# Performance work log

Measured on AMD Instinct MI355X. Metric: run time of the kernel, lower is better.

## Reference

```python
import jax, jax.numpy as jnp
import numpy as np

NUM_CAPS = 32
OUT_DIM = 8   # capsule vector length in channel terms; note the view() below mixes spatial dims
H_OUT = 6
W_OUT = 6


def setup_inputs() -> dict:
    key = jax.random.key(0)
    k1, k2, k3 = jax.random.split(key, 3)
    X = jax.random.normal(k1, (512, 256, 20, 20), dtype=jnp.float32)
    # 32 Conv2d(256->8, k=9) stacked capsule-major into one grouped-output conv
    W = jax.random.normal(k2, (256, 256, 9, 9), dtype=jnp.float32) * 0.02
    b = jax.random.normal(k3, (256,), dtype=jnp.float32) * 0.02
    return {"X": X, "W": W, "b": b}


def squash(u):
    # u: [B, 1152, 8]; squash along last dim (matches torch code exactly)
    ns = jnp.sum(u * u, axis=-1, keepdims=True)
    return ns / (1.0 + ns) * (u / (0.001 + jnp.sqrt(ns)))


def reference(X, W, b):
    # One conv replaces the 32 separate Conv2d modules; output channels are
    # ordered [cap0_ch0..cap0_ch7, cap1_ch0..], identical to torch.stack(dim=1)
    # followed by contiguous view.
    y = jax.lax.conv_general_dilated(
        X, W, window_strides=(2, 2), padding='VALID',
        dimension_numbers=('NCHW', 'OIHW', 'NCHW'))  # [B, 256, 6, 6]
    y = y + b[None, :, None, None]
    B = X.shape[0]
    # torch: stack -> [B,32,8,6,6] -> view(B, 32*36, -1) is a raw contiguous
    # reshape; [B,256,6,6] has the same memory layout, so reshape directly.
    u = y.reshape(B, NUM_CAPS * H_OUT * W_OUT, OUT_DIM)  # [B, 1152, 8]
    return squash(u)
```

## Files before the change

### kernel.cpp

```cpp
#include <hip/hip_runtime.h>
#include <hip/hip_bf16.h>
#include <stdint.h>

typedef __attribute__((ext_vector_type(8))) short bf16x8;
typedef __attribute__((ext_vector_type(4))) float f32x4;

__device__ __forceinline__ unsigned short f2bf(float f) {
  union { float f; unsigned int u; } v; v.f = f;
  unsigned int u = v.u;
  u += 0x7fffu + ((u >> 16) & 1u);
  return (unsigned short)(u >> 16);
}

__global__ __launch_bounds__(256) void xform_x(const float* __restrict__ X,
                                               unsigned short* __restrict__ Xt) {
  const int b = blockIdx.x;
  const int t = threadIdx.x;
  const float* src = X + ((size_t)b * 256 + t) * 400;
  unsigned short* dst = Xt + (size_t)b * 400 * 256 + t;
  for (int hw = 0; hw < 400; hw += 4) {
    float4 v = *(const float4*)(src + hw);
    dst[(size_t)(hw + 0) * 256] = f2bf(v.x);
    dst[(size_t)(hw + 1) * 256] = f2bf(v.y);
    dst[(size_t)(hw + 2) * 256] = f2bf(v.z);
    dst[(size_t)(hw + 3) * 256] = f2bf(v.w);
  }
}

__global__ __launch_bounds__(256) void xform_w(const float* __restrict__ W,
                                               unsigned short* __restrict__ Wt) {
  __shared__ unsigned short lds[81 * 128];
  const int co = blockIdx.x;
  const int ct = blockIdx.y;
  const int t = threadIdx.x;
  const float* src = W + ((size_t)co * 256 + (size_t)ct * 128) * 81;
  for (int idx = t; idx < 128 * 81; idx += 256) {
    int ci_l = idx / 81, khw = idx - ci_l * 81;
    lds[khw * 128 + ci_l] = f2bf(src[idx]);
  }
  __syncthreads();
  unsigned short* dst = Wt + (size_t)co * 256 + (size_t)ct * 128;
  for (int idx = t; idx < 81 * 128; idx += 256) {
    int khw = idx >> 7, ci_l = idx & 127;
    dst[(size_t)khw * 65536 + ci_l] = lds[idx];
  }
}

__device__ __forceinline__ void gload16(const unsigned short* g, unsigned short* l) {
  __builtin_amdgcn_global_load_lds(
      (const __attribute__((address_space(1))) unsigned int*)g,
      (__attribute__((address_space(3))) unsigned int*)l, 16, 0, 0);
}

__global__ __launch_bounds__(256, 2) void conv_gemm(
    const unsigned short* __restrict__ Xt,
    const unsigned short* __restrict__ Wt,
    const float* __restrict__ bias,
    float* __restrict__ Y) {
  __shared__ unsigned short sA[128 * 64];
  __shared__ unsigned short sB[64 * 64];
  const int mt = blockIdx.x;
  const int nt = blockIdx.y;
  const int t = threadIdx.x;
  const int c8 = t & 7, rq = t >> 3;
  const int swz = (c8 ^ (rq & 7)) * 8;

  int xb[4];
  #pragma unroll
  for (int r = 0; r < 4; ++r) {
    int m = mt * 128 + r * 32 + rq;
    int b = m / 36, s = m - b * 36;
    int oh = s / 6, ow = s - oh * 6;
    xb[r] = ((b * 20 + 2 * oh) * 20 + 2 * ow) * 256;
  }
  int wb[2];
  #pragma unroll
  for (int r = 0; r < 2; ++r) wb[r] = (nt * 64 + r * 32 + rq) * 256;

  unsigned short* ldsA = sA + t * 8;
  unsigned short* ldsB = sB + t * 8;

  const int lane = t & 63, wv = t >> 6;
  const int wm = (wv >> 1) * 64, wn = (wv & 1) * 32;
  const int l15 = lane & 15, l4 = lane >> 4, l7 = lane & 7;

  const unsigned short* pA[4][2];
  const unsigned short* pB[2][2];
  #pragma unroll
  for (int i = 0; i < 4; ++i)
    #pragma unroll
    for (int kk = 0; kk < 2; ++kk)
      pA[i][kk] = sA + ((wm + i * 16 + l15) * 128 +
                        ((kk * 64 + l4 * 16) ^ (l7 << 4))) / 2;
  #pragma unroll
  for (int j = 0; j < 2; ++j)
    #pragma unroll
    for (int kk = 0; kk < 2; ++kk)
      pB[j][kk] = sB + ((wn + j * 16 + l15) * 128 +
                        ((kk * 64 + l4 * 16) ^ (l7 << 4))) / 2;

  f32x4 acc[4][2];
  #pragma unroll
  for (int i = 0; i < 4; ++i)
    #pragma unroll
    for (int j = 0; j < 2; ++j) acc[i][j] = (f32x4){0.f, 0.f, 0.f, 0.f};

  #pragma unroll 1
  for (int kh = 0; kh < 9; ++kh) {
    #pragma unroll 1
    for (int kw = 0; kw < 9; ++kw) {
      const unsigned short* xsrc = Xt + (kh * 20 + kw) * 256 + swz;
      const unsigned short* wsrc = Wt + (kh * 9 + kw) * 65536 + swz;
      for (int ci0 = 0; ci0 < 256; ci0 += 64) {
        gload16(xsrc + xb[0] + ci0, ldsA + 0 * 2048);
        gload16(xsrc + xb[1] + ci0, ldsA + 1 * 2048);
        gload16(xsrc + xb[2] + ci0, ldsA + 2 * 2048);
        gload16(xsrc + xb[3] + ci0, ldsA + 3 * 2048);
        gload16(wsrc + wb[0] + ci0, ldsB + 0 * 2048);
        gload16(wsrc + wb[1] + ci0, ldsB + 1 * 2048);
        __syncthreads();
        bf16x8 af[4][2], bfr[2][2];
        #pragma unroll
        for (int i = 0; i < 4; ++i)
          #pragma unroll
          for (int kk = 0; kk < 2; ++kk) af[i][kk] = *(const bf16x8*)pA[i][kk];
        #pragma unroll
        for (int j = 0; j < 2; ++j)
          #pragma unroll
          for (int kk = 0; kk < 2; ++kk) bfr[j][kk] = *(const bf16x8*)pB[j][kk];
        #pragma unroll
        for (int i = 0; i < 4; ++i)
          #pragma unroll
          for (int j = 0; j < 2; ++j) {
            acc[i][j] = __builtin_amdgcn_mfma_f32_16x16x32_bf16(
                af[i][0], bfr[j][0], acc[i][j], 0, 0, 0);
            acc[i][j] = __builtin_amdgcn_mfma_f32_16x16x32_bf16(
                af[i][1], bfr[j][1], acc[i][j], 0, 0, 0);
          }
        __syncthreads();
      }
    }
  }

  #pragma unroll
  for (int j = 0; j < 2; ++j) {
    int co = nt * 64 + wn + j * 16 + l15;
    float bb = bias[co];
    #pragma unroll
    for (int i = 0; i < 4; ++i) {
      int m0 = mt * 128 + wm + i * 16 + l4 * 4;
      #pragma unroll
      for (int q = 0; q < 4; ++q) {
        int m = m0 + q;
        int b = m / 36, s = m - b * 36;
        Y[((size_t)b * 256 + co) * 36 + s] = acc[i][j][q] + bb;
      }
    }
  }
}

__global__ __launch_bounds__(256) void squash_k(float* __restrict__ Y) {
  const int g = blockIdx.x * 256 + threadIdx.x;
  float4* p = (float4*)(Y + (size_t)g * 8);
  float4 a = p[0], b = p[1];
  float ns = a.x * a.x + a.y * a.y + a.z * a.z + a.w * a.w +
             b.x * b.x + b.y * b.y + b.z * b.z + b.w * b.w;
  float sc = ns / ((1.0f + ns) * (0.001f + sqrtf(ns)));
  a.x *= sc; a.y *= sc; a.z *= sc; a.w *= sc;
  b.x *= sc; b.y *= sc; b.z *= sc; b.w *= sc;
  p[0] = a; p[1] = b;
}

extern "C" void kernel_launch(void* const* d_in, const int* in_sizes, int n_in,
                              void* d_out, int out_size, void* d_ws, size_t ws_size,
                              hipStream_t stream) {
  const float* X = (const float*)d_in[0];
  const float* W = (const float*)d_in[1];
  const float* bias = (const float*)d_in[2];
  float* Y = (float*)d_out;

  unsigned short* Xt = (unsigned short*)d_ws;
  unsigned short* Wt = Xt + (size_t)512 * 400 * 256;

  xform_x<<<512, 256, 0, stream>>>(X, Xt);
  xform_w<<<dim3(256, 2), 256, 0, stream>>>(W, Wt);
  conv_gemm<<<dim3(144, 4), 256, 0, stream>>>(Xt, Wt, bias, Y);
  squash_k<<<2304, 256, 0, stream>>>(Y);
}
```

Baseline: 385.0 us.

## Load A fragments directly to registers and double-buffer B in LDS

The conv GEMM no longer stages the activation tile in LDS. Each lane reads its A fragments straight from global memory into registers, which cuts LDS traffic and footprint. The weight tile is double-buffered in LDS and A registers are ping-ponged, so the next k-step's loads are issued before the current MFMAs run. The risk is uncoalesced direct global reads for A and higher register pressure under launch_bounds(256,2).

```diff
diff --git a/kernel.cpp b/kernel.cpp
--- a/kernel.cpp
+++ b/kernel.cpp
@@ -57,89 +57,102 @@
     const unsigned short* __restrict__ Wt,
     const float* __restrict__ bias,
     float* __restrict__ Y) {
-  __shared__ unsigned short sA[128 * 64];
-  __shared__ unsigned short sB[64 * 64];
+  __shared__ unsigned short sB[2 * 64 * 64];
   const int mt = blockIdx.x;
   const int nt = blockIdx.y;
   const int t = threadIdx.x;
   const int c8 = t & 7, rq = t >> 3;
   const int swz = (c8 ^ (rq & 7)) * 8;
 
-  int xb[4];
-  #pragma unroll
-  for (int r = 0; r < 4; ++r) {
-    int m = mt * 128 + r * 32 + rq;
-    int b = m / 36, s = m - b * 36;
-    int oh = s / 6, ow = s - oh * 6;
-    xb[r] = ((b * 20 + 2 * oh) * 20 + 2 * ow) * 256;
-  }
-  int wb[2];
-  #pragma unroll
-  for (int r = 0; r < 2; ++r) wb[r] = (nt * 64 + r * 32 + rq) * 256;
-
-  unsigned short* ldsA = sA + t * 8;
+  const int wb0 = (nt * 64 + rq) * 256 + swz;
+  const int wb1 = (nt * 64 + 32 + rq) * 256 + swz;
   unsigned short* ldsB = sB + t * 8;
 
   const int lane = t & 63, wv = t >> 6;
   const int wm = (wv >> 1) * 64, wn = (wv & 1) * 32;
   const int l15 = lane & 15, l4 = lane >> 4, l7 = lane & 7;
 
-  const unsigned short* pA[4][2];
-  const unsigned short* pB[2][2];
+  int arow[4];
+  #pragma unroll
+  for (int i = 0; i < 4; ++i) {
+    int m = mt * 128 + wm + i * 16 + l15;
+    int b = m / 36, s = m - b * 36;
+    int oh = s / 6, ow = s - oh * 6;
+    arow[i] = ((b * 20 + 2 * oh) * 20 + 2 * ow) * 256 + l4 * 8;
+  }
+
+  int pBo[2][2];
+  #pragma unroll
+  for (int j = 0; j < 2; ++j)
+    #pragma unroll
+    for (int kk = 0; kk < 2; ++kk)
+      pBo[j][kk] = ((wn + j * 16 + l15) * 128 +
+                    ((kk * 64 + l4 * 16) ^ (l7 << 4))) / 2;
+
+  f32x4 acc[4][2];
   #pragma unroll
   for (int i = 0; i < 4; ++i)
     #pragma unroll
-    for (int kk = 0; kk < 2; ++kk)
-      pA[i][kk] = sA + ((wm + i * 16 + l15) * 128 +
-                        ((kk * 64 + l4 * 16) ^ (l7 << 4))) / 2;
-  #pragma unroll
-  for (int j = 0; j < 2; ++j)
-    #pragma unroll
-    for (int kk = 0; kk < 2; ++kk)
-      pB[j][kk] = sB + ((wn + j * 16 + l15) * 128 +
-                        ((kk * 64 + l4 * 16) ^ (l7 << 4))) / 2;
-
-  f32x4 acc[4][2];
-  #pragma unroll
-  for (int i = 0; i < 4; ++i)
-    #pragma unroll
     for (int j = 0; j < 2; ++j) acc[i][j] = (f32x4){0.f, 0.f, 0.f, 0.f};
 
+  bf16x8 afA[4][2], afB[4][2];
+
+  int s_ci = 0, s_kw = 0, xo = 0, wo = 0;
+  auto adv = [&]() {
+    if (s_ci < 3) { ++s_ci; xo += 64; wo += 64; }
+    else {
+      s_ci = 0; wo += 65536 - 192;
+      if (s_kw < 8) { ++s_kw; xo += 64; }
+      else          { s_kw = 0; xo += 2880; }
+    }
+  };
+  auto loadA = [&](bf16x8 (&af)[4][2]) {
+    #pragma unroll
+    for (int i = 0; i < 4; ++i)
+      #pragma unroll
+      for (int kk = 0; kk < 2; ++kk)
+        af[i][kk] = *(const bf16x8*)(Xt + arow[i] + xo + kk * 32);
+  };
+  auto stageB = [&](int bufo) {
+    gload16(Wt + wo + wb0, ldsB + bufo);
+    gload16(Wt + wo + wb1, ldsB + bufo + 2048);
+  };
+  auto compute = [&](const unsigned short* base, bf16x8 (&af)[4][2]) {
+    bf16x8 bfr[2][2];
+    #pragma unroll
+    for (int j = 0; j < 2; ++j)
+      #pragma unroll
+      for (int kk = 0; kk < 2; ++kk)
+        bfr[j][kk] = *(const bf16x8*)(base + pBo[j][kk]);
+    #pragma unroll
+    for (int i = 0; i < 4; ++i)
+      #pragma unroll
+      for (int j = 0; j < 2; ++j) {
+        acc[i][j] = __builtin_amdgcn_mfma_f32_16x16x32_bf16(
+            af[i][0], bfr[j][0], acc[i][j], 0, 0, 0);
+        acc[i][j] = __builtin_amdgcn_mfma_f32_16x16x32_bf16(
+            af[i][1], bfr[j][1], acc[i][j], 0, 0, 0);
+      }
+  };
+
+  stageB(0);
+  loadA(afA);
+  adv();
+
   #pragma unroll 1
-  for (int kh = 0; kh < 9; ++kh) {
-    #pragma unroll 1
-    for (int kw = 0; kw < 9; ++kw) {
-      const unsigned short* xsrc = Xt + (kh * 20 + kw) * 256 + swz;
-      const unsigned short* wsrc = Wt + (kh * 9 + kw) * 65536 + swz;
-      for (int ci0 = 0; ci0 < 256; ci0 += 64) {
-        gload16(xsrc + xb[0] + ci0, ldsA + 0 * 2048);
-        gload16(xsrc + xb[1] + ci0, ldsA + 1 * 2048);
-        gload16(xsrc + xb[2] + ci0, ldsA + 2 * 2048);
-        gload16(xsrc + xb[3] + ci0, ldsA + 3 * 2048);
-        gload16(wsrc + wb[0] + ci0, ldsB + 0 * 2048);
-        gload16(wsrc + wb[1] + ci0, ldsB + 1 * 2048);
-        __syncthreads();
-        bf16x8 af[4][2], bfr[2][2];
-        #pragma unroll
-        for (int i = 0; i < 4; ++i)
-          #pragma unroll
-          for (int kk = 0; kk < 2; ++kk) af[i][kk] = *(const bf16x8*)pA[i][kk];
-        #pragma unroll
-        for (int j = 0; j < 2; ++j)
-          #pragma unroll
-          for (int kk = 0; kk < 2; ++kk) bfr[j][kk] = *(const bf16x8*)pB[j][kk];
-        #pragma unroll
-        for (int i = 0; i < 4; ++i)
-          #pragma unroll
-          for (int j = 0; j < 2; ++j) {
-            acc[i][j] = __builtin_amdgcn_mfma_f32_16x16x32_bf16(
-                af[i][0], bfr[j][0], acc[i][j], 0, 0, 0);
-            acc[i][j] = __builtin_amdgcn_mfma_f32_16x16x32_bf16(
-                af[i][1], bfr[j][1], acc[i][j], 0, 0, 0);
-          }
-        __syncthreads();
-      }
+  for (int s = 0; s < 324; s += 2) {
+    __syncthreads();
+    stageB(4096);
+    loadA(afB);
+    adv();
+    compute(sB, afA);
+    __syncthreads();
+    if (s + 2 < 324) {
+      stageB(0);
+      loadA(afA);
+      adv();
     }
+    compute(sB + 4096, afB);
   }
 
   #pragma unroll
```

Result: slower. 1.171 ms (+204.1%).

## Restructure conv GEMM with double-buffered LDS and intra-block split-K reduction

Applied to the files above, without the earlier changes.

Rewrites the conv GEMM main loop. It now uses a 64x128 tile with a K step of 32 and double-buffered LDS, so the global-to-LDS loads for the next step overlap with the MFMAs on the current one and one barrier per step replaces two. The four waves form two split-K halves over the flattened (kh, kw, ci) range. Their partial accumulators are reduced through LDS before bias is added and the result is stored. Launch bounds go to 3 blocks per CU and the grid becomes 288x2. The cost is extra LDS traffic for the reduction and a smaller K chunk per barrier.

```diff
diff --git a/kernel.cpp b/kernel.cpp
--- a/kernel.cpp
+++ b/kernel.cpp
@@ -52,108 +52,115 @@
       (__attribute__((address_space(3))) unsigned int*)l, 16, 0, 0);
 }
 
-__global__ __launch_bounds__(256, 2) void conv_gemm(
+__global__ __launch_bounds__(256, 3) void conv_gemm(
     const unsigned short* __restrict__ Xt,
     const unsigned short* __restrict__ Wt,
     const float* __restrict__ bias,
     float* __restrict__ Y) {
-  __shared__ unsigned short sA[128 * 64];
-  __shared__ unsigned short sB[64 * 64];
+  __shared__ __align__(16) unsigned short lds[2 * 12288];
   const int mt = blockIdx.x;
   const int nt = blockIdx.y;
   const int t = threadIdx.x;
-  const int c8 = t & 7, rq = t >> 3;
-  const int swz = (c8 ^ (rq & 7)) * 8;
+  const int l = t & 63, w = t >> 6;
+  const int wks = w >> 1;
+  const int l15 = l & 15, l4 = l >> 4;
+  const int sw = (l15 >> 1) & 3;
 
-  int xb[4];
+  int xsrcA[2], destA[2];
+  #pragma unroll
+  for (int r = 0; r < 2; ++r) {
+    int row = (w & 1) * 32 + r * 16 + (l >> 2);
+    int c4s = (l & 3) ^ ((row >> 1) & 3);
+    int m = mt * 64 + row;
+    int b = m / 36, sr = m - b * 36;
+    int oh = sr / 6, ow = sr - oh * 6;
+    xsrcA[r] = ((b * 20 + 2 * oh) * 20 + 2 * ow) * 256 + c4s * 8;
+    destA[r] = (w * 128 + r * 64 + l) * 8;
+  }
+  int wsrcB[4], destB[4];
   #pragma unroll
   for (int r = 0; r < 4; ++r) {
-    int m = mt * 128 + r * 32 + rq;
-    int b = m / 36, s = m - b * 36;
-    int oh = s / 6, ow = s - oh * 6;
-    xb[r] = ((b * 20 + 2 * oh) * 20 + 2 * ow) * 256;
+    int co = (w & 1) * 64 + r * 16 + (l >> 2);
+    int c4s = (l & 3) ^ ((co >> 1) & 3);
+    wsrcB[r] = (nt * 128 + co) * 256 + c4s * 8;
+    destB[r] = 4096 + (w * 256 + r * 64 + l) * 8;
   }
-  int wb[2];
-  #pragma unroll
-  for (int r = 0; r < 2; ++r) wb[r] = (nt * 64 + r * 32 + rq) * 256;
 
-  unsigned short* ldsA = sA + t * 8;
-  unsigned short* ldsB = sB + t * 8;
+  const int aoff = wks * 2048 + l15 * 32 + ((l4 ^ sw) * 8);
+  const int boff = 4096 + wks * 4096 + ((w & 1) * 64 + l15) * 32 + ((l4 ^ sw) * 8);
 
-  const int lane = t & 63, wv = t >> 6;
-  const int wm = (wv >> 1) * 64, wn = (wv & 1) * 32;
-  const int l15 = lane & 15, l4 = lane >> 4, l7 = lane & 7;
-
-  const unsigned short* pA[4][2];
-  const unsigned short* pB[2][2];
+  f32x4 acc[4][4];
   #pragma unroll
   for (int i = 0; i < 4; ++i)
     #pragma unroll
-    for (int kk = 0; kk < 2; ++kk)
-      pA[i][kk] = sA + ((wm + i * 16 + l15) * 128 +
-                        ((kk * 64 + l4 * 16) ^ (l7 << 4))) / 2;
-  #pragma unroll
-  for (int j = 0; j < 2; ++j)
+    for (int j = 0; j < 4; ++j) acc[i][j] = (f32x4){0.f, 0.f, 0.f, 0.f};
+
+  int xo, wo, ci, kw;
+  if (wks == 0) { xo = 0;     wo = 0;       ci = 0; kw = 0; }
+  else          { xo = 21632; wo = 2621568; ci = 4; kw = 4; }
+
+  auto adv = [&]() {
+    if (ci < 7) { ++ci; xo += 32; wo += 32; }
+    else { ci = 0; wo += 65312;
+           if (kw < 8) { ++kw; xo += 32; }
+           else        { kw = 0; xo += 2848; } }
+  };
+  auto stage = [&](int p) {
+    unsigned short* base = lds + p * 12288;
     #pragma unroll
-    for (int kk = 0; kk < 2; ++kk)
-      pB[j][kk] = sB + ((wn + j * 16 + l15) * 128 +
-                        ((kk * 64 + l4 * 16) ^ (l7 << 4))) / 2;
+    for (int r = 0; r < 2; ++r) gload16(Xt + xsrcA[r] + xo, base + destA[r]);
+    #pragma unroll
+    for (int r = 0; r < 4; ++r) gload16(Wt + wsrcB[r] + wo, base + destB[r]);
+  };
+  auto compute = [&](int p) {
+    const unsigned short* base = lds + p * 12288;
+    bf16x8 fa[4], fb[4];
+    #pragma unroll
+    for (int i = 0; i < 4; ++i) fa[i] = *(const bf16x8*)(base + aoff + i * 512);
+    #pragma unroll
+    for (int j = 0; j < 4; ++j) fb[j] = *(const bf16x8*)(base + boff + j * 512);
+    #pragma unroll
+    for (int i = 0; i < 4; ++i)
+      #pragma unroll
+      for (int j = 0; j < 4; ++j)
+        acc[i][j] = __builtin_amdgcn_mfma_f32_16x16x32_bf16(fa[i], fb[j],
+                                                            acc[i][j], 0, 0, 0);
+  };
 
-  f32x4 acc[4][2];
-  #pragma unroll
-  for (int i = 0; i < 4; ++i)
-    #pragma unroll
-    for (int j = 0; j < 2; ++j) acc[i][j] = (f32x4){0.f, 0.f, 0.f, 0.f};
-
+  stage(0); adv();
+  int p = 0;
   #pragma unroll 1
-  for (int kh = 0; kh < 9; ++kh) {
-    #pragma unroll 1
-    for (int kw = 0; kw < 9; ++kw) {
-      const unsigned short* xsrc = Xt + (kh * 20 + kw) * 256 + swz;
-      const unsigned short* wsrc = Wt + (kh * 9 + kw) * 65536 + swz;
-      for (int ci0 = 0; ci0 < 256; ci0 += 64) {
-        gload16(xsrc + xb[0] + ci0, ldsA + 0 * 2048);
-        gload16(xsrc + xb[1] + ci0, ldsA + 1 * 2048);
-        gload16(xsrc + xb[2] + ci0, ldsA + 2 * 2048);
-        gload16(xsrc + xb[3] + ci0, ldsA + 3 * 2048);
-        gload16(wsrc + wb[0] + ci0, ldsB + 0 * 2048);
-        gload16(wsrc + wb[1] + ci0, ldsB + 1 * 2048);
-        __syncthreads();
-        bf16x8 af[4][2], bfr[2][2];
-        #pragma unroll
-        for (int i = 0; i < 4; ++i)
-          #pragma unroll
-          for (int kk = 0; kk < 2; ++kk) af[i][kk] = *(const bf16x8*)pA[i][kk];
-        #pragma unroll
-        for (int j = 0; j < 2; ++j)
-          #pragma unroll
-          for (int kk = 0; kk < 2; ++kk) bfr[j][kk] = *(const bf16x8*)pB[j][kk];
-        #pragma unroll
-        for (int i = 0; i < 4; ++i)
-          #pragma unroll
-          for (int j = 0; j < 2; ++j) {
-            acc[i][j] = __builtin_amdgcn_mfma_f32_16x16x32_bf16(
-                af[i][0], bfr[j][0], acc[i][j], 0, 0, 0);
-            acc[i][j] = __builtin_amdgcn_mfma_f32_16x16x32_bf16(
-                af[i][1], bfr[j][1], acc[i][j], 0, 0, 0);
-          }
-        __syncthreads();
-      }
-    }
+  for (int s = 0; s < 324; ++s) {
+    __syncthreads();
+    if (s < 323) { stage(p ^ 1); adv(); }
+    compute(p);
+    p ^= 1;
   }
 
-  #pragma unroll
-  for (int j = 0; j < 2; ++j) {
-    int co = nt * 64 + wn + j * 16 + l15;
-    float bb = bias[co];
+  __syncthreads();
+  f32x4* red = (f32x4*)lds;
+  if (wks == 1) {
     #pragma unroll
-    for (int i = 0; i < 4; ++i) {
-      int m0 = mt * 128 + wm + i * 16 + l4 * 4;
+    for (int i = 0; i < 4; ++i)
       #pragma unroll
-      for (int q = 0; q < 4; ++q) {
-        int m = m0 + q;
-        int b = m / 36, s = m - b * 36;
-        Y[((size_t)b * 256 + co) * 36 + s] = acc[i][j][q] + bb;
+      for (int j = 0; j < 4; ++j)
+        red[(w & 1) * 1024 + (i * 4 + j) * 64 + l] = acc[i][j];
+  }
+  __syncthreads();
+  if (wks == 0) {
+    #pragma unroll
+    for (int j = 0; j < 4; ++j) {
+      int co = nt * 128 + (w & 1) * 64 + j * 16 + l15;
+      float bb = bias[co];
+      #pragma unroll
+      for (int i = 0; i < 4; ++i) {
+        f32x4 o = red[(w & 1) * 1024 + (i * 4 + j) * 64 + l];
+        #pragma unroll
+        for (int q = 0; q < 4; ++q) {
+          int m = mt * 64 + i * 16 + l4 * 4 + q;
+          int b = m / 36, sr = m - b * 36;
+          Y[((size_t)b * 256 + co) * 36 + sr] = acc[i][j][q] + o[q] + bb;
+        }
       }
     }
   }
@@ -184,6 +191,6 @@
 
   xform_x<<<512, 256, 0, stream>>>(X, Xt);
   xform_w<<<dim3(256, 2), 256, 0, stream>>>(W, Wt);
-  conv_gemm<<<dim3(144, 4), 256, 0, stream>>>(Xt, Wt, bias, Y);
+  conv_gemm<<<dim3(288, 2), 256, 0, stream>>>(Xt, Wt, bias, Y);
   squash_k<<<2304, 256, 0, stream>>>(Y);
 }
```

New measurement: 575.8 us. 1.5x slower.

## Double-buffer conv GEMM LDS tiles with async global-to-LDS prefetch

Applied to the files above, without the earlier changes.

The implicit-GEMM conv loop moves from a single LDS buffer with load-then-compute to a two-stage pipeline. It issues the global_load_lds for the next K step into the alternate buffer, then waits with vmcnt so only the current stage's loads must finish before computing. The nested kh/kw/ci loops are flattened into a 324-step loop with incremental offset updates, and s_setprio raises wave priority around the MFMA block. LDS use doubles to 48KB per block, which may limit occupancy at two blocks per CU.

```diff
diff --git a/kernel.cpp b/kernel.cpp
--- a/kernel.cpp
+++ b/kernel.cpp
@@ -57,8 +57,7 @@
     const unsigned short* __restrict__ Wt,
     const float* __restrict__ bias,
     float* __restrict__ Y) {
-  __shared__ unsigned short sA[128 * 64];
-  __shared__ unsigned short sB[64 * 64];
+  __shared__ __align__(16) unsigned short lds[2][12288];
   const int mt = blockIdx.x;
   const int nt = blockIdx.y;
   const int t = threadIdx.x;
@@ -71,33 +70,32 @@
     int m = mt * 128 + r * 32 + rq;
     int b = m / 36, s = m - b * 36;
     int oh = s / 6, ow = s - oh * 6;
-    xb[r] = ((b * 20 + 2 * oh) * 20 + 2 * ow) * 256;
+    xb[r] = ((b * 20 + 2 * oh) * 20 + 2 * ow) * 256 + swz;
   }
   int wb[2];
   #pragma unroll
-  for (int r = 0; r < 2; ++r) wb[r] = (nt * 64 + r * 32 + rq) * 256;
-
-  unsigned short* ldsA = sA + t * 8;
-  unsigned short* ldsB = sB + t * 8;
+  for (int r = 0; r < 2; ++r) wb[r] = (nt * 64 + r * 32 + rq) * 256 + swz;
+
+  const int dA = t * 8;
+  const int dB = 8192 + t * 8;
 
   const int lane = t & 63, wv = t >> 6;
   const int wm = (wv >> 1) * 64, wn = (wv & 1) * 32;
   const int l15 = lane & 15, l4 = lane >> 4, l7 = lane & 7;
 
-  const unsigned short* pA[4][2];
-  const unsigned short* pB[2][2];
+  int aOff[4][2], bOff[2][2];
   #pragma unroll
   for (int i = 0; i < 4; ++i)
     #pragma unroll
     for (int kk = 0; kk < 2; ++kk)
-      pA[i][kk] = sA + ((wm + i * 16 + l15) * 128 +
-                        ((kk * 64 + l4 * 16) ^ (l7 << 4))) / 2;
+      aOff[i][kk] = ((wm + i * 16 + l15) * 128 +
+                     ((kk * 64 + l4 * 16) ^ (l7 << 4))) / 2;
   #pragma unroll
   for (int j = 0; j < 2; ++j)
     #pragma unroll
     for (int kk = 0; kk < 2; ++kk)
-      pB[j][kk] = sB + ((wn + j * 16 + l15) * 128 +
-                        ((kk * 64 + l4 * 16) ^ (l7 << 4))) / 2;
+      bOff[j][kk] = 8192 + ((wn + j * 16 + l15) * 128 +
+                            ((kk * 64 + l4 * 16) ^ (l7 << 4))) / 2;
 
   f32x4 acc[4][2];
   #pragma unroll
@@ -105,41 +103,62 @@
     #pragma unroll
     for (int j = 0; j < 2; ++j) acc[i][j] = (f32x4){0.f, 0.f, 0.f, 0.f};
 
+  int s_ci = 0, s_kw = 0, xo = 0, wo = 0;
+  auto adv = [&]() {
+    if (s_ci < 3) { ++s_ci; xo += 64; wo += 64; }
+    else {
+      s_ci = 0; wo += 65536 - 192;
+      if (s_kw < 8) { ++s_kw; xo += 64; }
+      else          { s_kw = 0; xo += 2880; }
+    }
+  };
+  auto stage = [&](unsigned short* buf) {
+    #pragma unroll
+    for (int r = 0; r < 4; ++r) gload16(Xt + xb[r] + xo, buf + dA + r * 2048);
+    #pragma unroll
+    for (int r = 0; r < 2; ++r) gload16(Wt + wb[r] + wo, buf + dB + r * 2048);
+  };
+  auto compute = [&](const unsigned short* buf) {
+    bf16x8 af[4][2], bfr[2][2];
+    #pragma unroll
+    for (int i = 0; i < 4; ++i)
+      #pragma unroll
+      for (int kk = 0; kk < 2; ++kk) af[i][kk] = *(const bf16x8*)(buf + aOff[i][kk]);
+    #pragma unroll
+    for (int j = 0; j < 2; ++j)
+      #pragma unroll
+      for (int kk = 0; kk < 2; ++kk) bfr[j][kk] = *(const bf16x8*)(buf + bOff[j][kk]);
+    #pragma unroll
+    for (int i = 0; i < 4; ++i)
+      #pragma unroll
+      for (int j = 0; j < 2; ++j) {
+        acc[i][j] = __builtin_amdgcn_mfma_f32_16x16x32_bf16(
+            af[i][0], bfr[j][0], acc[i][j], 0, 0, 0);
+        acc[i][j] = __builtin_amdgcn_mfma_f32_16x16x32_bf16(
+            af[i][1], bfr[j][1], acc[i][j], 0, 0, 0);
+      }
+  };
+
+  stage(&lds[0][0]); adv();
+  int p = 0;
   #pragma unroll 1
-  for (int kh = 0; kh < 9; ++kh) {
-    #pragma unroll 1
-    for (int kw = 0; kw < 9; ++kw) {
-      const unsigned short* xsrc = Xt + (kh * 20 + kw) * 256 + swz;
-      const unsigned short* wsrc = Wt + (kh * 9 + kw) * 65536 + swz;
-      for (int ci0 = 0; ci0 < 256; ci0 += 64) {
-        gload16(xsrc + xb[0] + ci0, ldsA + 0 * 2048);
-        gload16(xsrc + xb[1] + ci0, ldsA + 1 * 2048);
-        gload16(xsrc + xb[2] + ci0, ldsA + 2 * 2048);
-        gload16(xsrc + xb[3] + ci0, ldsA + 3 * 2048);
-        gload16(wsrc + wb[0] + ci0, ldsB + 0 * 2048);
-        gload16(wsrc + wb[1] + ci0, ldsB + 1 * 2048);
-        __syncthreads();
-        bf16x8 af[4][2], bfr[2][2];
-        #pragma unroll
-        for (int i = 0; i < 4; ++i)
-          #pragma unroll
-          for (int kk = 0; kk < 2; ++kk) af[i][kk] = *(const bf16x8*)pA[i][kk];
-        #pragma unroll
-        for (int j = 0; j < 2; ++j)
-          #pragma unroll
-          for (int kk = 0; kk < 2; ++kk) bfr[j][kk] = *(const bf16x8*)pB[j][kk];
-        #pragma unroll
-        for (int i = 0; i < 4; ++i)
-          #pragma unroll
-          for (int j = 0; j < 2; ++j) {
-            acc[i][j] = __builtin_amdgcn_mfma_f32_16x16x32_bf16(
-                af[i][0], bfr[j][0], acc[i][j], 0, 0, 0);
-            acc[i][j] = __builtin_amdgcn_mfma_f32_16x16x32_bf16(
-                af[i][1], bfr[j][1], acc[i][j], 0, 0, 0);
-          }
-        __syncthreads();
-      }
+  for (int s = 0; s < 324; ++s) {
+    if (s < 323) {
+      stage(&lds[p ^ 1][0]); adv();
+      asm volatile("s_waitcnt vmcnt(6)" ::: "memory");
+    } else {
+      asm volatile("s_waitcnt vmcnt(0)" ::: "memory");
     }
+    __builtin_amdgcn_sched_barrier(0);
+    __builtin_amdgcn_s_barrier();
+    __builtin_amdgcn_sched_barrier(0);
+    __builtin_amdgcn_s_setprio(1);
+    compute(&lds[p][0]);
+    __builtin_amdgcn_s_setprio(0);
+    __builtin_amdgcn_sched_barrier(0);
+    __builtin_amdgcn_s_barrier();
+    __builtin_amdgcn_sched_barrier(0);
+    p ^= 1;
   }
 
   #pragma unroll
```

Result: slower. 505.4 us (+31.3%).
